# Optimization experiments

Measured on AMD Instinct MI355X. Metric: run time of the kernel, lower is better.

The kernel has to match this reference:

```python
import jax, jax.numpy as jnp
import numpy as np

N, E, D, K = 100000, 1600000, 32, 2
NEG_SLOPE = 0.01   # F.leaky_relu default
BN_EPS = 1e-5      # torch BatchNorm default


def setup_inputs() -> dict:
    key = jax.random.key(0)
    ks = jax.random.split(key, 8)
    y = jax.random.normal(ks[0], (N, D), jnp.float32)
    edge_index = jax.random.randint(ks[1], (2, E), 0, N, dtype=jnp.int32)
    edge_weight = jax.random.uniform(ks[2], (E,), jnp.float32)
    s = 1.0 / np.sqrt(D)
    # TAGConv(K=2): K+1 bias-free Linear(D,D) per layer, plus one output bias
    W1 = jax.random.uniform(ks[3], (K + 1, D, D), jnp.float32, -s, s)
    W2 = jax.random.uniform(ks[4], (K + 1, D, D), jnp.float32, -s, s)
    bias1 = jax.random.uniform(ks[5], (D,), jnp.float32, -s, s)
    bias2 = jax.random.uniform(ks[6], (D,), jnp.float32, -s, s)
    gamma1 = jnp.ones((D,), jnp.float32)
    beta1 = jnp.zeros((D,), jnp.float32)
    gamma2 = jnp.ones((D,), jnp.float32)
    beta2 = jnp.zeros((D,), jnp.float32)
    return dict(y=y, edge_index=edge_index, edge_weight=edge_weight,
                W1=W1, bias1=bias1, gamma1=gamma1, beta1=beta1,
                W2=W2, bias2=bias2, gamma2=gamma2, beta2=beta2)


def _tag_conv(x, W, b, src, dst, ew):
    # out = sum_{k=0..K} lin_k(A_w^k x) + bias, A_w: weighted sum-aggregation
    n = x.shape[0]
    out = x @ W[0]
    h = x
    for k in range(1, K + 1):
        msg = h[src] * ew[:, None]                         # [E, D] gather
        h = jax.ops.segment_sum(msg, dst, num_segments=n)  # scatter-add to targets
        out = out + h @ W[k]
    return out + b


def _batch_norm(x, gamma, beta):
    # training-mode BatchNorm over node dim, biased variance
    m = jnp.mean(x, axis=0)
    v = jnp.mean(jnp.square(x - m), axis=0)
    return (x - m) * jax.lax.rsqrt(v + BN_EPS) * gamma + beta


def reference(y, edge_index, edge_weight, W1, bias1, gamma1, beta1,
              W2, bias2, gamma2, beta2):
    src, dst = edge_index[0], edge_index[1]
    h = _tag_conv(y, W1, bias1, src, dst, edge_weight)
    h = jax.nn.leaky_relu(_batch_norm(h, gamma1, beta1), NEG_SLOPE)
    h = _tag_conv(h, W2, bias2, src, dst, edge_weight)
    h = jax.nn.leaky_relu(_batch_norm(h, gamma2, beta2), NEG_SLOPE)
    return h
```

## Files before the change

### kernel.cpp

```cpp
#include <hip/hip_runtime.h>

#define DD 32
#define NEG_SLOPE 0.01f
#define BN_EPS 1e-5f
#define SB 256

typedef unsigned short u16;
typedef unsigned int u32;

__device__ __forceinline__ u16 f32_to_bf16(float f) {
    u32 u = __float_as_uint(f);
    return (u16)((u + 0x7FFFu + ((u >> 16) & 1u)) >> 16);
}
__device__ __forceinline__ float bf16_to_f32(u16 b) {
    return __uint_as_float(((u32)b) << 16);
}


__global__ void zero_kernel(float* p, int n) {
    int i = blockIdx.x * blockDim.x + threadIdx.x;
    if (i < n) p[i] = 0.0f;
}
__global__ void zero_int_kernel(int* p, int n) {
    int i = blockIdx.x * blockDim.x + threadIdx.x;
    if (i < n) p[i] = 0;
}
__global__ void cvt_bf16_kernel(const float* __restrict__ x, u16* __restrict__ xb, int n) {
    int i = blockIdx.x * blockDim.x + threadIdx.x;
    if (i < n) xb[i] = f32_to_bf16(x[i]);
}


__global__ void hist_kernel(const int* dst, int* deg, int E) {
    int e = blockIdx.x * blockDim.x + threadIdx.x;
    if (e < E) atomicAdd(&deg[dst[e]], 1);
}

__global__ void scan_block_kernel(const int* deg, int* pre, int* bsum, int N) {
    __shared__ int sh[1024];
    int tid = threadIdx.x;
    int i = blockIdx.x * 1024 + tid;
    int v = (i < N) ? deg[i] : 0;
    sh[tid] = v;
    __syncthreads();
    for (int off = 1; off < 1024; off <<= 1) {
        int t = (tid >= off) ? sh[tid - off] : 0;
        __syncthreads();
        sh[tid] += t;
        __syncthreads();
    }
    if (i < N) pre[i] = sh[tid] - v;
    if (tid == 1023) bsum[blockIdx.x] = sh[1023];
}

__global__ void scan_sums_kernel(const int* bsum, int* boff, int nb) {
    __shared__ int sh[128];
    int tid = threadIdx.x;
    int v = (tid < nb) ? bsum[tid] : 0;
    sh[tid] = v;
    __syncthreads();
    for (int off = 1; off < 128; off <<= 1) {
        int t = (tid >= off) ? sh[tid - off] : 0;
        __syncthreads();
        sh[tid] += t;
        __syncthreads();
    }
    if (tid < nb) boff[tid] = sh[tid] - v;
}

__global__ void add_off_kernel(int* rowptr, int* cursor, const int* boff, int N, int E) {
    int i = blockIdx.x * blockDim.x + threadIdx.x;
    if (i < N) {
        int v = rowptr[i] + boff[i >> 10];
        rowptr[i] = v;
        cursor[i] = v;
    }
    if (i == 0) rowptr[N] = E;
}

__global__ void fill_kernel(const int* src, const int* dst, const float* ew,
                            int* cursor, int2* perm, int E) {
    int e = blockIdx.x * blockDim.x + threadIdx.x;
    if (e >= E) return;
    int p = atomicAdd(&cursor[dst[e]], 1);
    int2 q;
    q.x = src[e];
    q.y = __float_as_int(ew[e]);
    perm[p] = q;
}

template <bool EMIT>
__global__ void gather2_kernel(const u16* __restrict__ xb,
                               const int* __restrict__ rowptr,
                               const int2* __restrict__ perm,
                               float* __restrict__ out,
                               u16* __restrict__ outb, int N) {
    int t = blockIdx.x * blockDim.x + threadIdx.x;
    int n = t >> 6;
    if (n >= N) return;
    int lane = threadIdx.x & 63;
    int half = lane >> 5;
    int c = lane & 31;
    int b = rowptr[n], e = rowptr[n + 1];
    float a0 = 0.f, a1 = 0.f;
    int j = b + half;
    for (; j + 2 < e; j += 4) {
        int2 qa = perm[j];
        int2 qb = perm[j + 2];
        a0 += __int_as_float(qa.y) * bf16_to_f32(xb[qa.x * DD + c]);
        a1 += __int_as_float(qb.y) * bf16_to_f32(xb[qb.x * DD + c]);
    }
    if (j < e) {
        int2 q = perm[j];
        a0 += __int_as_float(q.y) * bf16_to_f32(xb[q.x * DD + c]);
    }
    float acc = a0 + a1;
    acc += __shfl_xor(acc, 32);
    if (half == 0) {
        out[n * DD + c] = acc;
        if (EMIT) outb[n * DD + c] = f32_to_bf16(acc);
    }
}

__global__ void combine_v3(const float* x0, const float* __restrict__ x1,
                           const float* __restrict__ x2, const float* __restrict__ W,
                           float* out, int N) {
    int c = threadIdx.x & 31;
    float w0[DD], w1[DD], w2[DD];
#pragma unroll
    for (int d = 0; d < DD; ++d) {
        w0[d] = W[d * DD + c];
        w1[d] = W[DD * DD + d * DD + c];
        w2[d] = W[2 * DD * DD + d * DD + c];
    }
    int group   = (blockIdx.x * blockDim.x + threadIdx.x) >> 5;
    int ngroups = (gridDim.x * blockDim.x) >> 5;
    for (int n = group; n < N; n += ngroups) {
        const float4* r0 = reinterpret_cast<const float4*>(x0 + (size_t)n * DD);
        const float4* r1 = reinterpret_cast<const float4*>(x1 + (size_t)n * DD);
        const float4* r2 = reinterpret_cast<const float4*>(x2 + (size_t)n * DD);
        float acc = 0.f;
#pragma unroll
        for (int q = 0; q < DD / 4; ++q) {
            float4 v0 = r0[q];
            float4 v1 = r1[q];
            float4 v2 = r2[q];
            acc += v0.x * w0[4*q] + v0.y * w0[4*q+1] + v0.z * w0[4*q+2] + v0.w * w0[4*q+3];
            acc += v1.x * w1[4*q] + v1.y * w1[4*q+1] + v1.z * w1[4*q+2] + v1.w * w1[4*q+3];
            acc += v2.x * w2[4*q] + v2.y * w2[4*q+1] + v2.z * w2[4*q+2] + v2.w * w2[4*q+3];
        }
        out[(size_t)n * DD + c] = acc;
    }
}


__global__ void stats_part_kernel(const float* x, float* part, int total) {
    int tid = threadIdx.x;
    int idx = blockIdx.x * 256 + tid;
    const int stride = SB * 256;
    float s = 0.f, ss = 0.f;
    for (int i = idx; i < total; i += stride) { float v = x[i]; s += v; ss += v * v; }
    __shared__ float sh[2][8][DD];
    sh[0][tid >> 5][tid & 31] = s;
    sh[1][tid >> 5][tid & 31] = ss;
    __syncthreads();
    if (tid < DD) {
        float ts = 0.f, tss = 0.f;
        for (int g = 0; g < 8; ++g) { ts += sh[0][g][tid]; tss += sh[1][g][tid]; }
        part[blockIdx.x * 64 + tid] = ts;
        part[blockIdx.x * 64 + DD + tid] = tss;
    }
}

__global__ void stats_final_kernel(const float* part, float* st) {
    int tid = threadIdx.x;
    if (tid < 64) {
        float a = 0.f;
        for (int b = 0; b < SB; ++b) a += part[b * 64 + tid];
        st[tid] = a;
    }
}

template <bool EMIT>
__global__ void bnrelu_kernel(const float* x, const float* stats,
                              const float* gamma, const float* beta,
                              float* out, u16* outb, int total, float invN) {
    int i = blockIdx.x * blockDim.x + threadIdx.x;
    if (i >= total) return;
    int c = i & 31;
    float m   = stats[c] * invN;
    float msq = stats[DD + c] * invN;
    float var = msq - m * m;
    float inv = 1.0f / sqrtf(var + BN_EPS);
    float v = (x[i] - m) * inv * gamma[c] + beta[c];
    v = v >= 0.f ? v : NEG_SLOPE * v;
    out[i] = v;
    if (EMIT) outb[i] = f32_to_bf16(v);
}


__global__ void prop_kernel(const float* x, const int* src, const int* dst,
                            const float* ew, float* out, int E) {
    int t = blockIdx.x * blockDim.x + threadIdx.x;
    int e = t >> 5;
    if (e >= E) return;
    int c = t & 31;
    float v = ew[e] * x[src[e] * DD + c];
    atomicAdd(&out[dst[e] * DD + c], v);
}

__global__ void combine_basic(const float* x0, const float* x1, const float* x2,
                              const float* W, const float* bias,
                              float* out, int N) {
    int t = blockIdx.x * blockDim.x + threadIdx.x;
    int n = t >> 5;
    if (n >= N) return;
    int c = t & 31;
    const float* r0 = x0 + n * DD;
    const float* r1 = x1 + n * DD;
    const float* r2 = x2 + n * DD;
    float acc = bias[c];
    for (int d = 0; d < DD; ++d) {
        acc += r0[d] * W[d * DD + c];
        acc += r1[d] * W[DD * DD + d * DD + c];
        acc += r2[d] * W[2 * DD * DD + d * DD + c];
    }
    out[t] = acc;
}

__global__ void stats_kernel(const float* x, float* stats, int N) {
    int c = blockIdx.x;
    int tid = threadIdx.x;
    float s = 0.f, ss = 0.f;
    for (int r = tid; r < N; r += 1024) {
        float v = x[r * DD + c];
        s += v; ss += v * v;
    }
    __shared__ float shs[1024];
    __shared__ float shq[1024];
    shs[tid] = s; shq[tid] = ss;
    __syncthreads();
    for (int off = 512; off > 0; off >>= 1) {
        if (tid < off) { shs[tid] += shs[tid + off]; shq[tid] += shq[tid + off]; }
        __syncthreads();
    }
    if (tid == 0) { stats[c] = shs[0]; stats[DD + c] = shq[0]; }
}


extern "C" void kernel_launch(void* const* d_in, const int* in_sizes, int n_in,
                              void* d_out, int out_size, void* d_ws, size_t ws_size,
                              hipStream_t stream) {
    const float* y   = (const float*)d_in[0];
    const int*   ei  = (const int*)d_in[1];
    const float* ew  = (const float*)d_in[2];
    const float* W1  = (const float*)d_in[3];
    const float* b1  = (const float*)d_in[4];
    const float* g1  = (const float*)d_in[5];
    const float* be1 = (const float*)d_in[6];
    const float* W2  = (const float*)d_in[7];
    const float* b2  = (const float*)d_in[8];
    const float* g2  = (const float*)d_in[9];
    const float* be2 = (const float*)d_in[10];
    float* out = (float*)d_out;

    const int N = in_sizes[0] / DD;
    const int E = in_sizes[2];
    const int total = N * DD;

    const int* src = ei;
    const int* dst = ei + E;

    const int RP = (N + 4) & ~3;
    float* st     = (float*)d_ws;
    float* h1     = st + 128;
    float* h2     = h1 + total;
    int*   rowptr = (int*)(h2 + total);
    int2*  perm   = (int2*)(rowptr + RP);
    u16*   h1b    = (u16*)(perm + E);
    float* part   = (float*)h1b;
    u16*   xb16   = (u16*)h2;

    const size_t tailBytes = ((size_t)total * 2 > (size_t)SB * 64 * 4)
                               ? (size_t)total * 2 : (size_t)SB * 64 * 4;
    const size_t need_bf16 = ((size_t)128 + 2 * (size_t)total + RP) * 4
                             + (size_t)E * 8 + tailBytes;
    const bool use_bf16 = ws_size >= need_bf16;

    int* cursor = (int*)h1;
    int* bsum   = (int*)h1 + N;
    int* boff   = bsum + 128;
    int* deg    = (int*)h2;

    const int NB = (N + 1023) / 1024;
    const float invN = 1.0f / (float)N;
    dim3 blk(256);
    const int ngrid = (N + 255) / 256;
    const int egrid = (E + 255) / 256;
    const int cgrid = (total + 255) / 256;
    const int ggrid = (2 * total + 255) / 256;
    const int zgrid = (2 * total + 255) / 256;
    const int pgrid = (E * DD + 255) / 256;
    const int vgrid = 1024;

    if (use_bf16) {
        zero_int_kernel<<<ngrid, blk, 0, stream>>>(deg, N);
        hist_kernel<<<egrid, blk, 0, stream>>>(dst, deg, E);
        scan_block_kernel<<<NB, 1024, 0, stream>>>(deg, rowptr, bsum, N);
        scan_sums_kernel<<<1, 128, 0, stream>>>(bsum, boff, NB);
        add_off_kernel<<<ngrid, blk, 0, stream>>>(rowptr, cursor, boff, N, E);
        fill_kernel<<<egrid, blk, 0, stream>>>(src, dst, ew, cursor, perm, E);

        cvt_bf16_kernel<<<cgrid, blk, 0, stream>>>(y, xb16, total);
        gather2_kernel<true><<<ggrid, blk, 0, stream>>>(xb16, rowptr, perm, h1, h1b, N);
        gather2_kernel<false><<<ggrid, blk, 0, stream>>>(h1b, rowptr, perm, h2, nullptr, N);
        combine_v3<<<vgrid, blk, 0, stream>>>(y, h1, h2, W1, out, N);
        stats_part_kernel<<<SB, blk, 0, stream>>>(out, part, total);
        stats_final_kernel<<<1, 64, 0, stream>>>(part, st);
        bnrelu_kernel<true><<<cgrid, blk, 0, stream>>>(out, st, g1, be1, out, xb16, total, invN);

        gather2_kernel<true><<<ggrid, blk, 0, stream>>>(xb16, rowptr, perm, h1, h1b, N);
        gather2_kernel<false><<<ggrid, blk, 0, stream>>>(h1b, rowptr, perm, h2, nullptr, N);
        combine_v3<<<vgrid, blk, 0, stream>>>(out, h1, h2, W2, out, N);
        stats_part_kernel<<<SB, blk, 0, stream>>>(out, part, total);
        stats_final_kernel<<<1, 64, 0, stream>>>(part, st + 64);
        bnrelu_kernel<false><<<cgrid, blk, 0, stream>>>(out, st + 64, g2, be2, out, nullptr, total, invN);
    } else {
        zero_kernel<<<zgrid, blk, 0, stream>>>(h1, 2 * total);
        prop_kernel<<<pgrid, blk, 0, stream>>>(y,  src, dst, ew, h1, E);
        prop_kernel<<<pgrid, blk, 0, stream>>>(h1, src, dst, ew, h2, E);
        combine_basic<<<cgrid, blk, 0, stream>>>(y, h1, h2, W1, b1, out, N);
        stats_kernel<<<32, 1024, 0, stream>>>(out, st, N);
        bnrelu_kernel<false><<<cgrid, blk, 0, stream>>>(out, st, g1, be1, out, nullptr, total, invN);

        zero_kernel<<<zgrid, blk, 0, stream>>>(h1, 2 * total);
        prop_kernel<<<pgrid, blk, 0, stream>>>(out, src, dst, ew, h1, E);
        prop_kernel<<<pgrid, blk, 0, stream>>>(h1,  src, dst, ew, h2, E);
        combine_basic<<<cgrid, blk, 0, stream>>>(out, h1, h2, W2, b2, out, N);
        stats_kernel<<<32, 1024, 0, stream>>>(out, st + 2 * DD, N);
        bnrelu_kernel<false><<<cgrid, blk, 0, stream>>>(out, st + 2 * DD, g2, be2, out, nullptr, total, invN);
    }
}
```

Before: 751.0 us.

## Build CSR via two-pass bucketed counting sort to localize scatter writes

Replaces the single-pass atomic fill of the CSR edge array with a two-level counting sort. Edges are first sharded into 128-node buckets using shared-memory counters and a transposed scan, then reordered within each bucket using per-node cursors. The aim is to turn random global scatter writes and atomics into mostly local ones. The cost is extra passes and kernel launches over the edges, plus a packing of src and local dst into one int that limits N to 2^20. The combine kernel also gets launch bounds.

```diff
diff --git a/kernel.cpp b/kernel.cpp
--- a/kernel.cpp
+++ b/kernel.cpp
@@ -4,6 +4,9 @@
 #define NEG_SLOPE 0.01f
 #define BN_EPS 1e-5f
 #define SB 256
+#define BKL 128
+#define EBLK 256
+#define MAXBUK 800
 
 typedef unsigned short u16;
 typedef unsigned int u32;
@@ -30,10 +33,19 @@
     if (i < n) xb[i] = f32_to_bf16(x[i]);
 }
 
-
-__global__ void hist_kernel(const int* dst, int* deg, int E) {
-    int e = blockIdx.x * blockDim.x + threadIdx.x;
-    if (e < E) atomicAdd(&deg[dst[e]], 1);
+__global__ void count_kernel(const int* __restrict__ dst, int* __restrict__ countsT,
+                             int E, int EPB, int NBUK) {
+    __shared__ int cnt[MAXBUK];
+    int eb = blockIdx.x;
+    for (int i = threadIdx.x; i < NBUK; i += blockDim.x) cnt[i] = 0;
+    __syncthreads();
+    int lo = eb * EPB;
+    int hi = lo + EPB; if (hi > E) hi = E;
+    for (int e = lo + threadIdx.x; e < hi; e += blockDim.x)
+        atomicAdd(&cnt[dst[e] >> 7], 1);
+    __syncthreads();
+    for (int i = threadIdx.x; i < NBUK; i += blockDim.x)
+        countsT[i * EBLK + eb] = cnt[i];
 }
 
 __global__ void scan_block_kernel(const int* deg, int* pre, int* bsum, int N) {
@@ -53,13 +65,13 @@
     if (tid == 1023) bsum[blockIdx.x] = sh[1023];
 }
 
-__global__ void scan_sums_kernel(const int* bsum, int* boff, int nb) {
-    __shared__ int sh[128];
+__global__ void scan_sums256(const int* bsum, int* boff, int nb) {
+    __shared__ int sh[256];
     int tid = threadIdx.x;
     int v = (tid < nb) ? bsum[tid] : 0;
     sh[tid] = v;
     __syncthreads();
-    for (int off = 1; off < 128; off <<= 1) {
+    for (int off = 1; off < 256; off <<= 1) {
         int t = (tid >= off) ? sh[tid - off] : 0;
         __syncthreads();
         sh[tid] += t;
@@ -68,6 +80,56 @@
     if (tid < nb) boff[tid] = sh[tid] - v;
 }
 
+__global__ void add_flat_kernel(int* a, const int* boff, int n) {
+    int i = blockIdx.x * blockDim.x + threadIdx.x;
+    if (i < n) a[i] += boff[i >> 10];
+}
+
+__global__ void shard_kernel(const int* __restrict__ src, const int* __restrict__ dst,
+                             const float* __restrict__ ew, const int* __restrict__ scanT,
+                             int2* __restrict__ perm2, int E, int EPB, int NBUK) {
+    __shared__ int cur[MAXBUK];
+    int eb = blockIdx.x;
+    for (int i = threadIdx.x; i < NBUK; i += blockDim.x)
+        cur[i] = scanT[i * EBLK + eb];
+    __syncthreads();
+    int lo = eb * EPB;
+    int hi = lo + EPB; if (hi > E) hi = E;
+    for (int e = lo + threadIdx.x; e < hi; e += blockDim.x) {
+        int d = dst[e];
+        int slot = atomicAdd(&cur[d >> 7], 1);
+        int2 q;
+        q.x = ((d & (BKL - 1)) << 20) | src[e];
+        q.y = __float_as_int(ew[e]);
+        perm2[slot] = q;
+    }
+}
+
+__global__ void reorder_kernel(const int2* __restrict__ perm2,
+                               const int* __restrict__ scanT,
+                               int* __restrict__ cursor,
+                               int2* __restrict__ perm, int E, int NBUK) {
+    int b = blockIdx.x;
+    int lo = scanT[b * EBLK];
+    int hi = (b + 1 < NBUK) ? scanT[(b + 1) * EBLK] : E;
+    int base = b * BKL;
+    for (int j = lo + threadIdx.x; j < hi; j += blockDim.x) {
+        int2 q = perm2[j];
+        int d = base + (q.x >> 20);
+        int slot = atomicAdd(&cursor[d], 1);
+        int2 o;
+        o.x = q.x & 0xFFFFF;
+        o.y = q.y;
+        perm[slot] = o;
+    }
+}
+
+
+__global__ void hist_kernel(const int* dst, int* deg, int E) {
+    int e = blockIdx.x * blockDim.x + threadIdx.x;
+    if (e < E) atomicAdd(&deg[dst[e]], 1);
+}
+
 __global__ void add_off_kernel(int* rowptr, int* cursor, const int* boff, int N, int E) {
     int i = blockIdx.x * blockDim.x + threadIdx.x;
     if (i < N) {
@@ -76,17 +138,6 @@
         cursor[i] = v;
     }
     if (i == 0) rowptr[N] = E;
-}
-
-__global__ void fill_kernel(const int* src, const int* dst, const float* ew,
-                            int* cursor, int2* perm, int E) {
-    int e = blockIdx.x * blockDim.x + threadIdx.x;
-    if (e >= E) return;
-    int p = atomicAdd(&cursor[dst[e]], 1);
-    int2 q;
-    q.x = src[e];
-    q.y = __float_as_int(ew[e]);
-    perm[p] = q;
 }
 
 template <bool EMIT>
@@ -122,9 +173,10 @@
     }
 }
 
-__global__ void combine_v3(const float* x0, const float* __restrict__ x1,
-                           const float* __restrict__ x2, const float* __restrict__ W,
-                           float* out, int N) {
+__global__ __launch_bounds__(256, 2)
+void combine_v3b(const float* x0, const float* __restrict__ x1,
+                 const float* __restrict__ x2, const float* __restrict__ W,
+                 float* out, int N) {
     int c = threadIdx.x & 31;
     float w0[DD], w1[DD], w2[DD];
 #pragma unroll
@@ -271,57 +323,72 @@
     const int* src = ei;
     const int* dst = ei + E;
 
+    const int NBUK = (N + BKL - 1) / BKL;
+    const int TOTC = NBUK * EBLK;
+    const int EPB  = (E + EBLK - 1) / EBLK;
+    const int NB2  = (TOTC + 1023) / 1024;
+    const int NB   = (N + 1023) / 1024;
+
     const int RP = (N + 4) & ~3;
     float* st     = (float*)d_ws;
     float* h1     = st + 128;
     float* h2     = h1 + total;
     int*   rowptr = (int*)(h2 + total);
     int2*  perm   = (int2*)(rowptr + RP);
-    u16*   h1b    = (u16*)(perm + E);
-    float* part   = (float*)h1b;
+    char*  tail   = (char*)(perm + E);
+    u16*   h1b    = (u16*)tail;
+    float* part   = (float*)tail;
+    int*   scanT  = (int*)tail;
+    int2*  perm2  = (int2*)h1;
     u16*   xb16   = (u16*)h2;
-
-    const size_t tailBytes = ((size_t)total * 2 > (size_t)SB * 64 * 4)
-                               ? (size_t)total * 2 : (size_t)SB * 64 * 4;
-    const size_t need_bf16 = ((size_t)128 + 2 * (size_t)total + RP) * 4
-                             + (size_t)E * 8 + tailBytes;
-    const bool use_bf16 = ws_size >= need_bf16;
-
-    int* cursor = (int*)h1;
-    int* bsum   = (int*)h1 + N;
-    int* boff   = bsum + 128;
-    int* deg    = (int*)h2;
-
-    const int NB = (N + 1023) / 1024;
+    int*   deg    = (int*)h2;
+    int*   cursor = deg + N;
+    int*   bsum   = deg + 2 * N;
+    int*   boff   = bsum + 256;
+
+    size_t tailBytes = (size_t)total * 2;
+    if ((size_t)SB * 64 * 4 > tailBytes) tailBytes = (size_t)SB * 64 * 4;
+    if ((size_t)TOTC * 4 > tailBytes)    tailBytes = (size_t)TOTC * 4;
+    const size_t need = ((size_t)128 + 2 * (size_t)total + RP + 2 * (size_t)E) * 4 + tailBytes;
+    const bool fast = (ws_size >= need) && (NBUK <= MAXBUK) && (N <= (1 << 20));
+
     const float invN = 1.0f / (float)N;
     dim3 blk(256);
     const int ngrid = (N + 255) / 256;
     const int egrid = (E + 255) / 256;
     const int cgrid = (total + 255) / 256;
     const int ggrid = (2 * total + 255) / 256;
+    const int fgrid = (TOTC + 255) / 256;
     const int zgrid = (2 * total + 255) / 256;
     const int pgrid = (E * DD + 255) / 256;
     const int vgrid = 1024;
 
-    if (use_bf16) {
+    if (fast) {
+        count_kernel<<<EBLK, blk, 0, stream>>>(dst, scanT, E, EPB, NBUK);
+        scan_block_kernel<<<NB2, 1024, 0, stream>>>(scanT, scanT, bsum, TOTC);
+        scan_sums256<<<1, 256, 0, stream>>>(bsum, boff, NB2);
+        add_flat_kernel<<<fgrid, blk, 0, stream>>>(scanT, boff, TOTC);
+        shard_kernel<<<EBLK, blk, 0, stream>>>(src, dst, ew, scanT, perm2, E, EPB, NBUK);
+
         zero_int_kernel<<<ngrid, blk, 0, stream>>>(deg, N);
         hist_kernel<<<egrid, blk, 0, stream>>>(dst, deg, E);
         scan_block_kernel<<<NB, 1024, 0, stream>>>(deg, rowptr, bsum, N);
-        scan_sums_kernel<<<1, 128, 0, stream>>>(bsum, boff, NB);
+        scan_sums256<<<1, 256, 0, stream>>>(bsum, boff, NB);
         add_off_kernel<<<ngrid, blk, 0, stream>>>(rowptr, cursor, boff, N, E);
-        fill_kernel<<<egrid, blk, 0, stream>>>(src, dst, ew, cursor, perm, E);
+
+        reorder_kernel<<<NBUK, blk, 0, stream>>>(perm2, scanT, cursor, perm, E, NBUK);
 
         cvt_bf16_kernel<<<cgrid, blk, 0, stream>>>(y, xb16, total);
         gather2_kernel<true><<<ggrid, blk, 0, stream>>>(xb16, rowptr, perm, h1, h1b, N);
         gather2_kernel<false><<<ggrid, blk, 0, stream>>>(h1b, rowptr, perm, h2, nullptr, N);
-        combine_v3<<<vgrid, blk, 0, stream>>>(y, h1, h2, W1, out, N);
+        combine_v3b<<<vgrid, blk, 0, stream>>>(y, h1, h2, W1, out, N);
         stats_part_kernel<<<SB, blk, 0, stream>>>(out, part, total);
         stats_final_kernel<<<1, 64, 0, stream>>>(part, st);
         bnrelu_kernel<true><<<cgrid, blk, 0, stream>>>(out, st, g1, be1, out, xb16, total, invN);
 
         gather2_kernel<true><<<ggrid, blk, 0, stream>>>(xb16, rowptr, perm, h1, h1b, N);
         gather2_kernel<false><<<ggrid, blk, 0, stream>>>(h1b, rowptr, perm, h2, nullptr, N);
-        combine_v3<<<vgrid, blk, 0, stream>>>(out, h1, h2, W2, out, N);
+        combine_v3b<<<vgrid, blk, 0, stream>>>(out, h1, h2, W2, out, N);
         stats_part_kernel<<<SB, blk, 0, stream>>>(out, part, total);
         stats_final_kernel<<<1, 64, 0, stream>>>(part, st + 64);
         bnrelu_kernel<false><<<cgrid, blk, 0, stream>>>(out, st + 64, g2, be2, out, nullptr, total, invN);
```

Result: faster. 660.5 us (-12.0%).
